# Kernel optimization log

Measured on AMD Instinct MI355X. Metric: run time of the kernel, lower is better.

Reference implementation:

```python
import jax, jax.numpy as jnp
import numpy as np
from jax import lax

HEADS = 8
DN = ('NCHW', 'OIHW', 'NCHW')


def setup_inputs() -> dict:
    key = jax.random.key(0)
    ks = jax.random.split(key, 7)
    B, C, H, W = 1, 256, 64, 64
    s = lambda k, shape, fan: jax.random.normal(k, shape, jnp.float32) / np.sqrt(fan)
    return {
        'x': jax.random.normal(ks[0], (B, C, H, W), jnp.float32),
        'w_qkv_pw': s(ks[1], (3 * C, C, 1, 1), C),
        'b_qkv_pw': jnp.zeros((3 * C,), jnp.float32),
        'w_qkv_dw': s(ks[2], (3 * C, 1, 11, 11), 121),
        'b_qkv_dw': jnp.zeros((3 * C,), jnp.float32),
        'w_lin': s(ks[3], (C, C, 1, 1), C),
        'b_lin': jnp.zeros((C,), jnp.float32),
    }


def reference(x, w_qkv_pw, b_qkv_pw, w_qkv_dw, b_qkv_dw, w_lin, b_lin):
    B, C, H, W = x.shape
    d = C // HEADS
    temp = float(int(np.sqrt(d)))  # matches int(math.sqrt(C // head)) in source

    # QKV: 1x1 conv then 11x11 depthwise conv (groups = 3C), padding 5
    qkv = lax.conv_general_dilated(x, w_qkv_pw, (1, 1), 'VALID', dimension_numbers=DN)
    qkv = qkv + b_qkv_pw[None, :, None, None]
    qkv = lax.conv_general_dilated(qkv, w_qkv_dw, (1, 1), [(5, 5), (5, 5)],
                                   dimension_numbers=DN, feature_group_count=3 * C)
    qkv = qkv + b_qkv_dw[None, :, None, None]

    q, k, v = jnp.split(qkv, 3, axis=1)  # each [B, C, H, W]
    N = H * W
    q = q.reshape(B, HEADS, d, N)
    k = k.reshape(B, HEADS, d, N)
    v = v.reshape(B, HEADS, d, N)

    # attn = softmax(q^T k / temp) over keys; [B, h, N, N]
    scores = jnp.einsum('bhdn,bhdm->bhnm', q, k) / temp
    attn = jax.nn.softmax(scores, axis=-1)
    out = jnp.einsum('bhnm,bhdm->bhdn', attn, v)  # [B, h, d, N]
    new_x = out.reshape(B, C, H, W)

    proj = lax.conv_general_dilated(new_x, w_lin, (1, 1), 'VALID', dimension_numbers=DN)
    proj = proj + b_lin[None, :, None, None]
    return jax.nn.relu(proj) + x
```

## Files before the change

kernel.cpp:

```cpp
#include <hip/hip_runtime.h>


typedef _Float16 f16;
typedef __fp16 hf16x2 __attribute__((ext_vector_type(2)));
typedef _Float16 f16x4 __attribute__((ext_vector_type(4)));
typedef _Float16 f16x8 __attribute__((ext_vector_type(8)));
typedef float f32x4 __attribute__((ext_vector_type(4)));

#define HW 4096
#define NC 256

#if __has_builtin(__builtin_amdgcn_exp2f)
#define EXP2(x) __builtin_amdgcn_exp2f(x)
#else
#define EXP2(x) exp2f(x)
#endif

static __device__ __forceinline__ f32x4 mfma16(f16x8 a, f16x8 b, f32x4 c) {
  return __builtin_amdgcn_mfma_f32_16x16x32_f16(a, b, c, 0, 0, 0);
}

static __device__ __forceinline__ void gload16(const void* g, void* l) {
  __builtin_amdgcn_global_load_lds(
      (const __attribute__((address_space(1))) unsigned int*)g,
      (__attribute__((address_space(3))) unsigned int*)l, 16, 0, 0);
}

__global__ __launch_bounds__(256) void k_prep(
    const float* __restrict__ x, f16* __restrict__ xt,
    const float* __restrict__ wpw, const float* __restrict__ wlin,
    f16* __restrict__ wpw_h, f16* __restrict__ wlin_h,
    int* __restrict__ kmax_bits) {
  __shared__ float t[32][33];
  int b = blockIdx.x;
  if (b < 1024) {
    int bc = b >> 7;
    int bp = b & 127;
    int tx = threadIdx.x & 31, ty = threadIdx.x >> 5;
#pragma unroll
    for (int i = 0; i < 4; i++) {
      int c = bc * 32 + ty + i * 8;
      t[ty + i * 8][tx] = x[c * HW + bp * 32 + tx];
    }
    __syncthreads();
#pragma unroll
    for (int i = 0; i < 4; i++) {
      int p = bp * 32 + ty + i * 8;
      xt[p * NC + bc * 32 + tx] = (f16)t[tx][ty + i * 8];
    }
  } else {
    int i = (b - 1024) * 256 + threadIdx.x;
    if (i < 8) kmax_bits[i] = 0;
    for (int idx = i; idx < 3 * NC * NC; idx += 32768)
      wpw_h[idx] = (f16)wpw[idx];
    for (int idx = i; idx < NC * NC; idx += 32768)
      wlin_h[idx] = (f16)wlin[idx];
  }
}

__global__ __launch_bounds__(256) void k_gemm_qkv(
    const f16* __restrict__ w, const f16* __restrict__ xt,
    const float* __restrict__ bias, f16* __restrict__ out) {
  __shared__ f16 lds_b[64 * 256];
  int bm = blockIdx.x >> 6;
  int bn = blockIdx.x & 63;
  int tid = threadIdx.x;
  int wave = tid >> 6, lane = tid & 63;
  int r = lane & 15, g = lane >> 4;
  int m0 = bm * 128 + wave * 32;
  int n0 = bn * 64;
#pragma unroll
  for (int round = 0; round < 8; ++round) {
    int idx = round * 256 + tid;
    int row = idx >> 5;
    int sd = (idx & 31) ^ (row & 7);
    gload16(xt + (n0 + row) * 256 + sd * 8,
            (char*)lds_b + round * 4096 + wave * 1024);
  }
  __syncthreads();
  f32x4 acc[2][4] = {};
  for (int kk = 0; kk < NC; kk += 32) {
    f16x8 a0 = *(const f16x8*)&w[(m0 + r) * NC + kk + g * 8];
    f16x8 a1 = *(const f16x8*)&w[(m0 + 16 + r) * NC + kk + g * 8];
    int sb = (kk >> 3) + g;
#pragma unroll
    for (int nt = 0; nt < 4; nt++) {
      int row = nt * 16 + r;
      f16x8 bfr = *(const f16x8*)((char*)lds_b + row * 512 +
                                  ((sb ^ (row & 7)) * 16));
      acc[0][nt] = mfma16(a0, bfr, acc[0][nt]);
      acc[1][nt] = mfma16(a1, bfr, acc[1][nt]);
    }
  }
#pragma unroll
  for (int mg = 0; mg < 2; mg++) {
    int mbase = m0 + mg * 16 + g * 4;
    float bj[4];
#pragma unroll
    for (int j = 0; j < 4; j++) bj[j] = bias[mbase + j];
#pragma unroll
    for (int nt = 0; nt < 4; nt++)
#pragma unroll
      for (int j = 0; j < 4; j++)
        out[(mbase + j) * HW + n0 + nt * 16 + r] =
            (f16)(acc[mg][nt][j] + bj[j]);
  }
}

__global__ __launch_bounds__(256) void k_dwconv(
    const f16* __restrict__ qkv, const float* __restrict__ wdw,
    const float* __restrict__ bdw, f16* __restrict__ q_nm,
    f16* __restrict__ k_nm, f16* __restrict__ v_cm) {
  __shared__ float img[42 * 74];
  __shared__ float wgt[121];
  int b = blockIdx.x;
  int c = b >> 1, half = b & 1;
  int y0 = half * 32;
  int tid = threadIdx.x;
  for (int i = tid; i < 420; i += 256) {
    int row = i / 10, cc = i - row * 10;
    img[row * 74 + (cc < 5 ? cc : 64 + cc)] = 0.f;
  }
  const f16x8 zv = {};
  for (int task = tid; task < 336; task += 256) {
    int row = task >> 3, ch = task & 7;
    int y = y0 + row - 5;
    f16x8 v = ((unsigned)y < 64u)
                  ? *(const f16x8*)&qkv[c * HW + y * 64 + ch * 8]
                  : zv;
    float* dst = &img[row * 74 + 5 + ch * 8];
#pragma unroll
    for (int j = 0; j < 8; j++) dst[j] = (float)v[j];
  }
  for (int i = tid; i < 121; i += 256) wgt[i] = wdw[c * 121 + i];
  __syncthreads();
  float bias = bdw[c];
  int px0 = half * 2048 + tid * 8;
  int yl = tid >> 3;
  int x0 = (tid & 7) * 8;
  float acc[8] = {};
#pragma unroll
  for (int ky = 0; ky < 11; ky++) {
    const float* rp = &img[(yl + ky) * 74 + x0];
    float rv[18];
#pragma unroll
    for (int t = 0; t < 18; t++) rv[t] = rp[t];
#pragma unroll
    for (int kx = 0; kx < 11; kx++) {
      float wv = wgt[ky * 11 + kx];
#pragma unroll
      for (int p = 0; p < 8; p++) acc[p] = fmaf(rv[kx + p], wv, acc[p]);
    }
  }
  if (c < 256) {
    int h = c >> 5, d = c & 31;
#pragma unroll
    for (int p = 0; p < 8; p++)
      q_nm[(h * HW + px0 + p) * 32 + d] =
          (f16)((acc[p] + bias) * 0.28853900817779268f);
  } else if (c < 512) {
    int cc = c - 256;
    int h = cc >> 5, d = cc & 31;
#pragma unroll
    for (int p = 0; p < 8; p++)
      k_nm[(h * HW + px0 + p) * 32 + d] = (f16)(acc[p] + bias);
  } else {
    int cc = c - 512;
#pragma unroll
    for (int p = 0; p < 8; p++)
      v_cm[cc * HW + px0 + p] = (f16)(acc[p] + bias);
  }
}

__global__ __launch_bounds__(256) void k_norms(
    const f16* __restrict__ q_nm, const f16* __restrict__ k_nm,
    float* __restrict__ q_bound, int* __restrict__ kmax_bits) {
  __shared__ float red[256];
  int b = blockIdx.x, t = threadIdx.x;
  const f16* src = (b < 128) ? q_nm : k_nm;
  int row = ((b & 127) * 256) + t;
  const f16x8* p = (const f16x8*)&src[row * 32];
  float s = 0.f;
#pragma unroll
  for (int i = 0; i < 4; i++) {
    f16x8 v = p[i];
#pragma unroll
    for (int j = 0; j < 8; j++) {
      float f = (float)v[j];
      s = fmaf(f, f, s);
    }
  }
  float nrm = sqrtf(s);
  if (b < 128) {
    q_bound[row] = nrm;
  } else {
    red[t] = nrm;
    __syncthreads();
    for (int off = 128; off > 0; off >>= 1) {
      if (t < off) red[t] = fmaxf(red[t], red[t + off]);
      __syncthreads();
    }
    if (t == 0) atomicMax(&kmax_bits[row >> 12], __float_as_int(red[0]));
  }
}

__global__ __launch_bounds__(512, 4) void k_attn(
    const f16* __restrict__ q_nm, const f16* __restrict__ k_nm,
    const f16* __restrict__ v_cm, const float* __restrict__ q_bound,
    const int* __restrict__ kmax_bits, f16* __restrict__ o_part,
    float* __restrict__ l_part) {
  __shared__ f16 lds_k[4][2048];
  __shared__ f16 lds_v[4][2048];
  int bid = blockIdx.x;
  int h = bid & 7, kq = (bid >> 3) & 3, qt = bid >> 5;
  int tid = threadIdx.x;
  int wv = tid >> 6, lane = tid & 63;
  int r = lane & 15, g = lane >> 4;
  int n_base = qt * 256 + wv * 32;
  int m_lo = kq << 10;
  const f16* qh = q_nm + h * (HW * 32);
  const f16* kh = k_nm + h * (HW * 32) + m_lo * 32;
  const f16* vh = v_cm + h * (32 * HW) + m_lo;

  f16x8 bq0 = *(const f16x8*)&qh[(n_base + r) * 32 + g * 8];
  f16x8 bq1 = *(const f16x8*)&qh[(n_base + 16 + r) * 32 + g * 8];
  float kmax = __int_as_float(kmax_bits[h]);
  float mCa = 13.9f - q_bound[h * HW + n_base + r] * kmax;
  float mCb = 13.9f - q_bound[h * HW + n_base + 16 + r] * kmax;
  f32x4 cinitA = {mCa, mCa, mCa, mCa};
  f32x4 cinitB = {mCb, mCb, mCb, mCb};
  int pr = ((r & 12) << 1) | (r & 3);
  f32x4 accA0 = {0.f, 0.f, 0.f, 0.f}, accA1 = {0.f, 0.f, 0.f, 0.f};
  f32x4 accB0 = {0.f, 0.f, 0.f, 0.f}, accB1 = {0.f, 0.f, 0.f, 0.f};
  float La = 0.f, Lb = 0.f;

  int l4 = lane >> 2, l3 = lane & 3;
  int kc = (wv & 3) * 16 + l4;
  int ku = (kc >> 3) & 3;
  const f16* kg_base = kh + kc * 32 + (l3 ^ ku) * 8;
  int t2v = (tid >= 256) ? tid - 256 : 0;
  int vd = t2v >> 3;
  int vkk = ((t2v & 7) ^ (vd & 7)) * 8;
  const f16* vg_base = vh + vd * HW + vkk;
  f16* kdst = &lds_k[0][0] + (wv & 3) * 512;
  f16* vdst = &lds_v[0][0] + (t2v >> 6) * 512;

  int u = r >> 2;
  int kslot = ((g ^ u) & 3) * 16;
  int ak0_off = pr * 64 + kslot;
  int ak1_off = (pr + 4) * 64 + kslot;
  int vb_off0 = (r * 128 + g * 16) ^ ((r & 7) << 4);
  int vb_off1 = (r * 128 + 64 + g * 16) ^ ((r & 7) << 4);

  __builtin_amdgcn_s_waitcnt(0);
  if (wv < 4) {
    gload16(kg_base, kdst);
    gload16(kg_base + 2048, kdst + 2048);
  } else {
    gload16(vg_base, vdst);
    gload16(vg_base + 64, vdst + 2048);
  }

  for (int t = 0; t < 16; ++t) {
    int c2 = (t + 2 <= 15) ? t + 2 : 15;
    int b2 = (t + 2) & 3;
    if (wv < 4)
      gload16(kg_base + c2 * 2048, kdst + b2 * 2048);
    else
      gload16(vg_base + c2 * 64, vdst + b2 * 2048);
    asm volatile("s_waitcnt vmcnt(2)" ::: "memory");
    __builtin_amdgcn_sched_barrier(0);
    __builtin_amdgcn_s_barrier();
    __builtin_amdgcn_sched_barrier(0);
    const char* kb = (const char*)&lds_k[t & 3][0];
    const char* vb = (const char*)&lds_v[t & 3][0];
#pragma unroll
    for (int ks = 0; ks < 2; ++ks) {
      f16x8 ak0 = *(const f16x8*)(kb + ks * 2048 + ak0_off);
      f16x8 ak1 = *(const f16x8*)(kb + ks * 2048 + ak1_off);
      int vo = ks ? vb_off1 : vb_off0;
      f16x8 bv0 = *(const f16x8*)(vb + vo);
      f16x8 bv1 = *(const f16x8*)(vb + vo + 2048);
      __builtin_amdgcn_s_setprio(1);
      f32x4 sA0 = mfma16(ak0, bq0, cinitA);
      f32x4 sA1 = mfma16(ak1, bq0, cinitA);
      f32x4 sB0 = mfma16(ak0, bq1, cinitB);
      f32x4 sB1 = mfma16(ak1, bq1, cinitB);
      __builtin_amdgcn_s_setprio(0);
      float pA[8], pB[8];
#pragma unroll
      for (int j = 0; j < 4; j++) {
        pA[j] = EXP2(sA0[j]);
        pA[4 + j] = EXP2(sA1[j]);
        pB[j] = EXP2(sB0[j]);
        pB[4 + j] = EXP2(sB1[j]);
      }
      La += ((pA[0] + pA[1]) + (pA[2] + pA[3])) +
            ((pA[4] + pA[5]) + (pA[6] + pA[7]));
      Lb += ((pB[0] + pB[1]) + (pB[2] + pB[3])) +
            ((pB[4] + pB[5]) + (pB[6] + pB[7]));
      union { hf16x2 h2[4]; f16x8 v; } uA, uB;
#pragma unroll
      for (int j = 0; j < 4; j++) {
        uA.h2[j] = __builtin_amdgcn_cvt_pkrtz(pA[2 * j], pA[2 * j + 1]);
        uB.h2[j] = __builtin_amdgcn_cvt_pkrtz(pB[2 * j], pB[2 * j + 1]);
      }
      __builtin_amdgcn_s_setprio(1);
      accA0 = mfma16(uA.v, bv0, accA0);
      accA1 = mfma16(uA.v, bv1, accA1);
      accB0 = mfma16(uB.v, bv0, accB0);
      accB1 = mfma16(uB.v, bv1, accB1);
      __builtin_amdgcn_s_setprio(0);
    }
  }
  La += __shfl_xor(La, 16);
  La += __shfl_xor(La, 32);
  Lb += __shfl_xor(Lb, 16);
  Lb += __shfl_xor(Lb, 32);
  float ilA = 1.f / La, ilB = 1.f / Lb;
  f16* op = o_part + ((((size_t)kq * 8 + h) * HW) + n_base) * 32;
#pragma unroll
  for (int j = 0; j < 4; j++) {
    float ija = __shfl(ilA, 4 * g + j);
    float ijb = __shfl(ilB, 4 * g + j);
    op[(4 * g + j) * 32 + r] = (f16)(accA0[j] * ija);
    op[(4 * g + j) * 32 + 16 + r] = (f16)(accA1[j] * ija);
    op[(16 + 4 * g + j) * 32 + r] = (f16)(accB0[j] * ijb);
    op[(16 + 4 * g + j) * 32 + 16 + r] = (f16)(accB1[j] * ijb);
  }
  if (lane < 16) {
    l_part[(((size_t)kq * 8 + h) * HW) + n_base + r] = La;
    l_part[(((size_t)kq * 8 + h) * HW) + n_base + 16 + r] = Lb;
  }
}

__global__ __launch_bounds__(256) void k_norm_o(
    const f16* __restrict__ o_part, const float* __restrict__ l_part,
    f16* __restrict__ nx) {
  int idx = blockIdx.x * 256 + threadIdx.x;
  int h = idx >> 15, row = (idx >> 3) & (HW - 1), d0 = (idx & 7) * 4;
  size_t rbase = ((size_t)h * HW) + row;
  float Lq[4];
  f16x4 oq[4];
#pragma unroll
  for (int q = 0; q < 4; q++) {
    Lq[q] = l_part[(size_t)q * 8 * HW + rbase];
    oq[q] = *(const f16x4*)&o_part[((size_t)q * 8 * HW + rbase) * 32 + d0];
  }
  float inv = 1.f / (((Lq[0] + Lq[1]) + (Lq[2] + Lq[3])));
  f16x4 out;
#pragma unroll
  for (int j = 0; j < 4; j++) {
    float o = 0.f;
#pragma unroll
    for (int q = 0; q < 4; q++) o = fmaf((float)oq[q][j], Lq[q], o);
    out[j] = (f16)(o * inv);
  }
  *(f16x4*)&nx[row * NC + h * 32 + d0] = out;
}

__global__ __launch_bounds__(256) void k_gemm_proj(
    const f16* __restrict__ w, const f16* __restrict__ nx,
    const float* __restrict__ bias, const float* __restrict__ x,
    float* __restrict__ out) {
  __shared__ f16 lds_b[32 * 256];
  int bm = blockIdx.x >> 7;
  int bn = blockIdx.x & 127;
  int tid = threadIdx.x;
  int wave = tid >> 6, lane = tid & 63;
  int r = lane & 15, g = lane >> 4;
  int m_row = bm * 64 + wave * 16 + r;
  int n0 = bn * 32;
#pragma unroll
  for (int round = 0; round < 4; ++round) {
    int idx = round * 256 + tid;
    int row = idx >> 5;
    int sd = (idx & 31) ^ (row & 7);
    gload16(nx + (n0 + row) * 256 + sd * 8,
            (char*)lds_b + round * 4096 + wave * 1024);
  }
  __syncthreads();
  f32x4 acc[2] = {};
  for (int kk = 0; kk < NC; kk += 32) {
    f16x8 a = *(const f16x8*)&w[m_row * NC + kk + g * 8];
    int sb = (kk >> 3) + g;
#pragma unroll
    for (int nt = 0; nt < 2; nt++) {
      int row = nt * 16 + r;
      f16x8 bfr = *(const f16x8*)((char*)lds_b + row * 512 +
                                  ((sb ^ (row & 7)) * 16));
      acc[nt] = mfma16(a, bfr, acc[nt]);
    }
  }
  int mbase = bm * 64 + wave * 16 + g * 4;
  float bj[4];
#pragma unroll
  for (int j = 0; j < 4; j++) bj[j] = bias[mbase + j];
#pragma unroll
  for (int nt = 0; nt < 2; nt++)
#pragma unroll
    for (int j = 0; j < 4; j++) {
      int m = mbase + j, n = n0 + nt * 16 + r;
      float v = fmaxf(acc[nt][j] + bj[j], 0.f) + x[m * HW + n];
      out[m * HW + n] = v;
    }
}

extern "C" void kernel_launch(void* const* d_in, const int* in_sizes, int n_in,
                              void* d_out, int out_size, void* d_ws,
                              size_t ws_size, hipStream_t stream) {
  const float* x = (const float*)d_in[0];
  const float* w_pw = (const float*)d_in[1];
  const float* b_pw = (const float*)d_in[2];
  const float* w_dw = (const float*)d_in[3];
  const float* b_dw = (const float*)d_in[4];
  const float* w_lin = (const float*)d_in[5];
  const float* b_lin = (const float*)d_in[6];
  float* out = (float*)d_out;

  char* ws = (char*)d_ws;
  f16* wpw_h = (f16*)(ws + 0);
  f16* wlin_h = (f16*)(ws + 393216);
  f16* xt = (f16*)(ws + 524288);
  f16* qkv = (f16*)(ws + 2621440);
  f16* q_nm = (f16*)(ws + 15204352);
  f16* k_nm = (f16*)(ws + 17301504);
  f16* v_cm = (f16*)(ws + 19398656);
  f16* nx = (f16*)(ws + 21495808);
  float* q_bound = (float*)(ws + 23592960);
  int* kmax_bits = (int*)(ws + 23724032);
  f16* o_part = (f16*)(ws + 2621440);
  float* l_part = (float*)(ws + 2621440 + 8388608);

  k_prep<<<1152, 256, 0, stream>>>(x, xt, w_pw, w_lin, wpw_h, wlin_h,
                                   kmax_bits);
  k_gemm_qkv<<<384, 256, 0, stream>>>(wpw_h, xt, b_pw, qkv);
  k_dwconv<<<1536, 256, 0, stream>>>(qkv, w_dw, b_dw, q_nm, k_nm, v_cm);
  k_norms<<<256, 256, 0, stream>>>(q_nm, k_nm, q_bound, kmax_bits);
  k_attn<<<512, 512, 0, stream>>>(q_nm, k_nm, v_cm, q_bound, kmax_bits,
                                  o_part, l_part);
  k_norm_o<<<1024, 256, 0, stream>>>(o_part, l_part, nx);
  k_gemm_proj<<<512, 256, 0, stream>>>(wlin_h, nx, b_lin, x, out);
}
```

Baseline: 82.13 us.

## Fuse partial-output combine into projection GEMM and compute Q norms inside attention

Removes the k_norm_o kernel by having the projection GEMM load the four key-split partial outputs and their row sums, combine and normalise them, and write the result straight into shared memory instead of going through the nx buffer. The q norm bound is now computed inside the attention kernel from the Q fragments already in registers, using cross-lane shuffles, so k_norms only handles K and launches half as many blocks. This saves one launch and a global round trip for nx and q_bound. In exchange, the four GEMM blocks sharing each column tile (one per bm) now redo the combine, and the LDS fill becomes synchronous register stores instead of asynchronous global-to-LDS loads.

```diff
diff --git a/kernel.cpp b/kernel.cpp
--- a/kernel.cpp
+++ b/kernel.cpp
@@ -173,13 +173,11 @@
 }
 
 __global__ __launch_bounds__(256) void k_norms(
-    const f16* __restrict__ q_nm, const f16* __restrict__ k_nm,
-    float* __restrict__ q_bound, int* __restrict__ kmax_bits) {
+    const f16* __restrict__ k_nm, int* __restrict__ kmax_bits) {
   __shared__ float red[256];
   int b = blockIdx.x, t = threadIdx.x;
-  const f16* src = (b < 128) ? q_nm : k_nm;
-  int row = ((b & 127) * 256) + t;
-  const f16x8* p = (const f16x8*)&src[row * 32];
+  int row = b * 256 + t;
+  const f16x8* p = (const f16x8*)&k_nm[row * 32];
   float s = 0.f;
 #pragma unroll
   for (int i = 0; i < 4; i++) {
@@ -190,25 +188,19 @@
       s = fmaf(f, f, s);
     }
   }
-  float nrm = sqrtf(s);
-  if (b < 128) {
-    q_bound[row] = nrm;
-  } else {
-    red[t] = nrm;
+  red[t] = sqrtf(s);
+  __syncthreads();
+  for (int off = 128; off > 0; off >>= 1) {
+    if (t < off) red[t] = fmaxf(red[t], red[t + off]);
     __syncthreads();
-    for (int off = 128; off > 0; off >>= 1) {
-      if (t < off) red[t] = fmaxf(red[t], red[t + off]);
-      __syncthreads();
-    }
-    if (t == 0) atomicMax(&kmax_bits[row >> 12], __float_as_int(red[0]));
-  }
+  }
+  if (t == 0) atomicMax(&kmax_bits[row >> 12], __float_as_int(red[0]));
 }
 
 __global__ __launch_bounds__(512, 4) void k_attn(
     const f16* __restrict__ q_nm, const f16* __restrict__ k_nm,
-    const f16* __restrict__ v_cm, const float* __restrict__ q_bound,
-    const int* __restrict__ kmax_bits, f16* __restrict__ o_part,
-    float* __restrict__ l_part) {
+    const f16* __restrict__ v_cm, const int* __restrict__ kmax_bits,
+    f16* __restrict__ o_part, float* __restrict__ l_part) {
   __shared__ f16 lds_k[4][2048];
   __shared__ f16 lds_v[4][2048];
   int bid = blockIdx.x;
@@ -224,9 +216,20 @@
 
   f16x8 bq0 = *(const f16x8*)&qh[(n_base + r) * 32 + g * 8];
   f16x8 bq1 = *(const f16x8*)&qh[(n_base + 16 + r) * 32 + g * 8];
+  float s2a = 0.f, s2b = 0.f;
+#pragma unroll
+  for (int j = 0; j < 8; j++) {
+    float fa = (float)bq0[j], fb = (float)bq1[j];
+    s2a = fmaf(fa, fa, s2a);
+    s2b = fmaf(fb, fb, s2b);
+  }
+  s2a += __shfl_xor(s2a, 16);
+  s2a += __shfl_xor(s2a, 32);
+  s2b += __shfl_xor(s2b, 16);
+  s2b += __shfl_xor(s2b, 32);
   float kmax = __int_as_float(kmax_bits[h]);
-  float mCa = 13.9f - q_bound[h * HW + n_base + r] * kmax;
-  float mCb = 13.9f - q_bound[h * HW + n_base + 16 + r] * kmax;
+  float mCa = 13.9f - sqrtf(s2a) * kmax;
+  float mCb = 13.9f - sqrtf(s2b) * kmax;
   f32x4 cinitA = {mCa, mCa, mCa, mCa};
   f32x4 cinitB = {mCb, mCb, mCb, mCb};
   int pr = ((r & 12) << 1) | (r & 3);
@@ -334,35 +337,10 @@
   }
 }
 
-__global__ __launch_bounds__(256) void k_norm_o(
-    const f16* __restrict__ o_part, const float* __restrict__ l_part,
-    f16* __restrict__ nx) {
-  int idx = blockIdx.x * 256 + threadIdx.x;
-  int h = idx >> 15, row = (idx >> 3) & (HW - 1), d0 = (idx & 7) * 4;
-  size_t rbase = ((size_t)h * HW) + row;
-  float Lq[4];
-  f16x4 oq[4];
-#pragma unroll
-  for (int q = 0; q < 4; q++) {
-    Lq[q] = l_part[(size_t)q * 8 * HW + rbase];
-    oq[q] = *(const f16x4*)&o_part[((size_t)q * 8 * HW + rbase) * 32 + d0];
-  }
-  float inv = 1.f / (((Lq[0] + Lq[1]) + (Lq[2] + Lq[3])));
-  f16x4 out;
-#pragma unroll
-  for (int j = 0; j < 4; j++) {
-    float o = 0.f;
-#pragma unroll
-    for (int q = 0; q < 4; q++) o = fmaf((float)oq[q][j], Lq[q], o);
-    out[j] = (f16)(o * inv);
-  }
-  *(f16x4*)&nx[row * NC + h * 32 + d0] = out;
-}
-
 __global__ __launch_bounds__(256) void k_gemm_proj(
-    const f16* __restrict__ w, const f16* __restrict__ nx,
-    const float* __restrict__ bias, const float* __restrict__ x,
-    float* __restrict__ out) {
+    const f16* __restrict__ w, const f16* __restrict__ o_part,
+    const float* __restrict__ l_part, const float* __restrict__ bias,
+    const float* __restrict__ x, float* __restrict__ out) {
   __shared__ f16 lds_b[32 * 256];
   int bm = blockIdx.x >> 7;
   int bn = blockIdx.x & 127;
@@ -373,11 +351,27 @@
   int n0 = bn * 32;
 #pragma unroll
   for (int round = 0; round < 4; ++round) {
-    int idx = round * 256 + tid;
-    int row = idx >> 5;
-    int sd = (idx & 31) ^ (row & 7);
-    gload16(nx + (n0 + row) * 256 + sd * 8,
-            (char*)lds_b + round * 4096 + wave * 1024);
+    int task = round * 256 + tid;
+    int row = task >> 5, grp = task & 31;
+    int h = grp >> 2, d0 = (grp & 3) * 8;
+    size_t rbase = ((size_t)h * HW) + n0 + row;
+    float Lq[4];
+    f16x8 oq[4];
+#pragma unroll
+    for (int q = 0; q < 4; q++) {
+      Lq[q] = l_part[(size_t)q * 8 * HW + rbase];
+      oq[q] = *(const f16x8*)&o_part[((size_t)q * 8 * HW + rbase) * 32 + d0];
+    }
+    float inv = 1.f / ((Lq[0] + Lq[1]) + (Lq[2] + Lq[3]));
+    f16x8 outv;
+#pragma unroll
+    for (int j = 0; j < 8; j++) {
+      float o = 0.f;
+#pragma unroll
+      for (int q = 0; q < 4; q++) o = fmaf((float)oq[q][j], Lq[q], o);
+      outv[j] = (f16)(o * inv);
+    }
+    *(f16x8*)((char*)lds_b + row * 512 + ((grp ^ (row & 7)) * 16)) = outv;
   }
   __syncthreads();
   f32x4 acc[2] = {};
@@ -426,8 +420,6 @@
   f16* q_nm = (f16*)(ws + 15204352);
   f16* k_nm = (f16*)(ws + 17301504);
   f16* v_cm = (f16*)(ws + 19398656);
-  f16* nx = (f16*)(ws + 21495808);
-  float* q_bound = (float*)(ws + 23592960);
   int* kmax_bits = (int*)(ws + 23724032);
   f16* o_part = (f16*)(ws + 2621440);
   float* l_part = (float*)(ws + 2621440 + 8388608);
@@ -436,9 +428,8 @@
                                    kmax_bits);
   k_gemm_qkv<<<384, 256, 0, stream>>>(wpw_h, xt, b_pw, qkv);
   k_dwconv<<<1536, 256, 0, stream>>>(qkv, w_dw, b_dw, q_nm, k_nm, v_cm);
-  k_norms<<<256, 256, 0, stream>>>(q_nm, k_nm, q_bound, kmax_bits);
-  k_attn<<<512, 512, 0, stream>>>(q_nm, k_nm, v_cm, q_bound, kmax_bits,
-                                  o_part, l_part);
-  k_norm_o<<<1024, 256, 0, stream>>>(o_part, l_part, nx);
-  k_gemm_proj<<<512, 256, 0, stream>>>(wlin_h, nx, b_lin, x, out);
-}
+  k_norms<<<128, 256, 0, stream>>>(k_nm, kmax_bits);
+  k_attn<<<512, 512, 0, stream>>>(q_nm, k_nm, v_cm, kmax_bits, o_part,
+                                  l_part);
+  k_gemm_proj<<<512, 256, 0, stream>>>(wlin_h, o_part, l_part, b_lin, x, out);
+}
```

Result: no change. 82.80 us (+0.8%).
